# Performance work log

Measured on AMD Instinct MI355X. Metric: run time of the kernel, lower is better.

## Reference

```python
import jax, jax.numpy as jnp
import numpy as np

D = 16      # stroke_embedding_dim
H = 2       # num_heads
DH = D // H # head dim = 8
HID = 32    # hidden_dim
OUT = 32    # output_dim
N = 250000  # num edge nodes
F = 500000  # num faces
E = 4       # edges per face


def setup_inputs() -> dict:
    key = jax.random.key(0)
    ks = jax.random.split(key, 10)
    s = 1.0 / np.sqrt(D)
    return {
        "node_embed": jax.random.normal(ks[0], (1, N, D), dtype=jnp.float32),
        "face_edge_ids": jax.random.randint(ks[1], (F, E), 0, N),
        # nn.MultiheadAttention in_proj (packed q,k,v) and out_proj, stored [in, out]
        "w_in": jax.random.uniform(ks[2], (D, 3 * D), jnp.float32, -s, s),
        "b_in": jnp.zeros((3 * D,), jnp.float32),
        "w_out": jax.random.uniform(ks[3], (D, D), jnp.float32, -s, s),
        "b_out": jnp.zeros((D,), jnp.float32),
        # fc: Linear(16 -> 32), fc_output: Linear(32 -> 32)
        "fc_w": jax.random.uniform(ks[4], (D, HID), jnp.float32, -s, s),
        "fc_b": jax.random.uniform(ks[5], (HID,), jnp.float32, -s, s),
        "fco_w": jax.random.uniform(ks[6], (HID, OUT), jnp.float32, -1 / np.sqrt(HID), 1 / np.sqrt(HID)),
        "fco_b": jax.random.uniform(ks[7], (OUT,), jnp.float32, -1 / np.sqrt(HID), 1 / np.sqrt(HID)),
    }


def reference(node_embed, face_edge_ids, w_in, b_in, w_out, b_out, fc_w, fc_b, fco_w, fco_b):
    # Gather per-face edge embeddings: [F, E, D]
    x = node_embed[0][face_edge_ids]
    # Packed qkv projection
    qkv = x @ w_in + b_in                                  # [F, E, 3D]
    q, k, v = jnp.split(qkv, 3, axis=-1)
    def heads(t):
        return t.reshape(F, E, H, DH).transpose(0, 2, 1, 3)  # [F, H, E, DH]
    q, k, v = heads(q), heads(k), heads(v)
    scores = jnp.einsum("fhqd,fhkd->fhqk", q, k) / np.sqrt(DH)
    attn = jax.nn.softmax(scores, axis=-1)
    o = jnp.einsum("fhqk,fhkd->fhqd", attn, v)             # [F, H, E, DH]
    o = o.transpose(0, 2, 1, 3).reshape(F, E, D)
    attn_out = o @ w_out + b_out                           # [F, E, D]
    h = jax.nn.relu(attn_out @ fc_w + fc_b)                # [F, E, HID]
    pooled = h.mean(axis=1)                                # [F, HID]
    out = pooled @ fco_w + fco_b                           # [F, OUT]
    return out[None]                                       # [1, F, OUT]
```

## Files before the change

kernel.cpp:

```cpp
#include <hip/hip_runtime.h>
#include <stdint.h>


typedef float v2f __attribute__((ext_vector_type(2)));
typedef _Float16 v2h __attribute__((ext_vector_type(2)));
typedef __fp16 h4 __attribute__((ext_vector_type(4)));
typedef float f32x4 __attribute__((ext_vector_type(4)));
typedef uint32_t u32x2 __attribute__((ext_vector_type(2)));
typedef uint32_t u32x4 __attribute__((ext_vector_type(4)));

#define DPP_ROT1 0x39
#define DPP_ROT2 0x4E
#define DPP_ROT3 0x93
#define DPP_XOR1 0xB1

template<int CTRL>
static __device__ __forceinline__ float dppf(float x) {
    return __builtin_bit_cast(float,
        __builtin_amdgcn_mov_dpp(__builtin_bit_cast(int, x), CTRL, 0xF, 0xF, true));
}
template<int CTRL>
static __device__ __forceinline__ v2h dpph(v2h x) {
    return __builtin_bit_cast(v2h,
        __builtin_amdgcn_mov_dpp(__builtin_bit_cast(int, x), CTRL, 0xF, 0xF, true));
}

static __device__ __forceinline__ v2h pkh(float a, float b) {
    v2h r; r.x = (_Float16)a; r.y = (_Float16)b; return r;
}
static __device__ __forceinline__ v2h pkrtz(float a, float b) {
#if __has_builtin(__builtin_amdgcn_cvt_pkrtz)
    return __builtin_bit_cast(v2h, __builtin_amdgcn_cvt_pkrtz(a, b));
#else
    return pkh(a, b);
#endif
}
static __device__ __forceinline__ float fdot2(v2h a, v2h b, float c) {
#if __has_builtin(__builtin_amdgcn_fdot2)
    return __builtin_amdgcn_fdot2(a, b, c, false);
#else
    return fmaf((float)a.x, (float)b.x, fmaf((float)a.y, (float)b.y, c));
#endif
}
static __device__ __forceinline__ v2h fmah(v2h a, v2h b, v2h c) {
    return __builtin_elementwise_fma(a, b, c);
}
static __device__ __forceinline__ v2h ash(uint32_t u) {
    return __builtin_bit_cast(v2h, u);
}
static __device__ __forceinline__ uint32_t bcu(v2h h) {
    return __builtin_bit_cast(uint32_t, h);
}
static __device__ __forceinline__ h4 mkh4(uint32_t lo, uint32_t hi) {
    u32x2 t; t.x = lo; t.y = hi; return __builtin_bit_cast(h4, t);
}
static __device__ __forceinline__ h4 ld2h(const uint32_t* p) {
    u32x2 t; t.x = p[0]; t.y = p[1]; return __builtin_bit_cast(h4, t);
}
static __device__ __forceinline__ f32x4 mfma16(h4 a, h4 b, f32x4 c) {
    return __builtin_amdgcn_mfma_f32_16x16x16f16(a, b, c, 0, 0, 0);
}

template<int CTRL>
static __device__ __forceinline__ void score_rot(const v2h* qh, const v2h* kh,
                                                 float& r0, float& r1) {
    float a0 = 0.f, a1 = 0.f;
#pragma unroll
    for (int d = 0; d < 4; ++d) {
        a0 = fdot2(qh[d],     dpph<CTRL>(kh[d]),     a0);
        a1 = fdot2(qh[4 + d], dpph<CTRL>(kh[4 + d]), a1);
    }
    r0 = a0; r1 = a1;
}
template<int CTRL>
static __device__ __forceinline__ void pv_rot(const v2h* vh, v2h ps0, v2h ps1,
                                              v2h* o) {
#pragma unroll
    for (int d = 0; d < 8; ++d) {
        const v2h vr = dpph<CTRL>(vh[d]);
        o[d] = fmah(d < 4 ? ps0 : ps1, vr, o[d]);
    }
}

static __device__ __forceinline__ void xchg_store(uint32_t* S, int a, int c0,
                                                  int g2, f32x4 c) {
    const float p0 = dppf<DPP_XOR1>(c[0]);
    const float p1 = dppf<DPP_XOR1>(c[1]);
    const float p2 = dppf<DPP_XOR1>(c[2]);
    const float p3 = dppf<DPP_XOR1>(c[3]);
    if ((c0 & 1) == 0) {
        u32x4 w;
        w.x = bcu(pkrtz(c[0], p0));
        w.y = bcu(pkrtz(c[1], p1));
        w.z = bcu(pkrtz(c[2], p2));
        w.w = bcu(pkrtz(c[3], p3));
        *reinterpret_cast<u32x4*>(S + ((c0 >> 1) * 68 + 16 * a + 4 * g2)) = w;
    }
}

__global__ void fold_w(const float* __restrict__ w_in,
                       const float* __restrict__ w_out,
                       const float* __restrict__ b_out,
                       const float* __restrict__ fc_w,
                       const float* __restrict__ fc_b,
                       const float* __restrict__ fco_w,
                       uint32_t* __restrict__ wsu) {
    const int tid = threadIdx.x;
    if (blockIdx.x == 0) {
        if (tid < 384) {
            const int T = tid >> 7, r = tid & 127, l = r >> 1, d = r & 1;
            const int o = 16 * T + (l & 15), k0 = 4 * (l >> 4) + 2 * d;
            wsu[tid] = bcu(pkh(w_in[k0 * 48 + o], w_in[(k0 + 1) * 48 + o]));
        } else if (tid < 640) {
            const int i = tid - 384, b = i >> 7, r = i & 127, l = r >> 1, d = r & 1;
            const int c = 16 * b + (l & 15), k0 = 4 * (l >> 4) + 2 * d;
            float a0 = 0.f, a1 = 0.f;
#pragma unroll
            for (int e = 0; e < 16; ++e) {
                a0 = fmaf(w_out[k0 * 16 + e],       fc_w[e * 32 + c], a0);
                a1 = fmaf(w_out[(k0 + 1) * 16 + e], fc_w[e * 32 + c], a1);
            }
            wsu[tid] = bcu(pkh(a0, a1));
        }
    } else {
        if (tid < 32) {
            float acc = fc_b[tid];
#pragma unroll
            for (int e = 0; e < 16; ++e)
                acc = fmaf(b_out[e], fc_w[e * 32 + tid], acc);
            reinterpret_cast<float*>(wsu)[640 + tid] = acc;
        } else if (tid < 544) {
            const int i = tid - 32;
            const int kt = i >> 8, n = (i >> 7) & 1, r = i & 127, l = r >> 1, d = r & 1;
            const int col = 16 * n + (l & 15), k0 = 16 * kt + 4 * (l >> 4) + 2 * d;
            wsu[672 + i] = bcu(pkh(fco_w[k0 * 32 + col] * 0.25f,
                                   fco_w[(k0 + 1) * 32 + col] * 0.25f));
        }
    }
}

__launch_bounds__(256, 4)
__global__ void face_net(const float* __restrict__ node,
                         const int*   __restrict__ fids,
                         const float* __restrict__ b_in,
                         const uint32_t* __restrict__ wsu,
                         const float* __restrict__ fco_b,
                         float* __restrict__ out, int F) {
    const int l   = threadIdx.x & 63;
    const int wid = threadIdx.x >> 6;
    const int token_base = blockIdx.x * 256 + wid * 64;
    if (token_base >= 4 * F) return;
    const int c0 = l & 15, g2 = l >> 4;

    __shared__ __align__(16) uint8_t lds[4 * 4736];
    uint8_t* wl = lds + wid * 4736;
    uint32_t* S0 = reinterpret_cast<uint32_t*>(wl);
    uint32_t* S1 = reinterpret_cast<uint32_t*>(wl + 2176);

    h4 A[4];
#pragma unroll
    for (int a = 0; a < 4; ++a) {
        const int tok = token_base + 16 * a + c0;
        const int nid = fids[tok];
        const float4 xv = *reinterpret_cast<const float4*>(
            node + (size_t)nid * 16 + g2 * 4);
        A[a] = mkh4(bcu(pkrtz(xv.x, xv.y)), bcu(pkrtz(xv.z, xv.w)));
    }

    const h4 Bq = ld2h(wsu + 0   + l * 2);
    const h4 Bk = ld2h(wsu + 128 + l * 2);
    const float bq = b_in[c0];
    {
        const f32x4 cq0 = {bq, bq, bq, bq};
        const f32x4 ck0 = {0.f, 0.f, 0.f, 0.f};
#pragma unroll
        for (int a = 0; a < 4; ++a) xchg_store(S0, a, c0, g2, mfma16(A[a], Bq, cq0));
#pragma unroll
        for (int a = 0; a < 4; ++a) xchg_store(S1, a, c0, g2, mfma16(A[a], Bk, ck0));
    }

    v2h qh[8], kh[8];
#pragma unroll
    for (int u = 0; u < 4; ++u) {
        qh[2 * u]     = ash(S0[(2 * u) * 68 + l]);
        qh[2 * u + 1] = ash(S0[(2 * u + 1) * 68 + l]);
        kh[2 * u]     = ash(S1[(2 * u) * 68 + l]);
        kh[2 * u + 1] = ash(S1[(2 * u + 1) * 68 + l]);
    }

    float p0[4], p1[4];
    {
        float a0 = 0.f, a1 = 0.f;
#pragma unroll
        for (int d = 0; d < 4; ++d) {
            a0 = fdot2(qh[d], kh[d], a0);
            a1 = fdot2(qh[4 + d], kh[4 + d], a1);
        }
        p0[0] = a0; p1[0] = a1;
    }
    score_rot<DPP_ROT1>(qh, kh, p0[1], p1[1]);
    score_rot<DPP_ROT2>(qh, kh, p0[2], p1[2]);
    score_rot<DPP_ROT3>(qh, kh, p0[3], p1[3]);

    {
        const float C = 0.51006974841f;
        float s0 = 0.f, s1 = 0.f;
#pragma unroll
        for (int j = 0; j < 4; ++j) {
            p0[j] = __builtin_amdgcn_exp2f(p0[j] * C); s0 += p0[j];
            p1[j] = __builtin_amdgcn_exp2f(p1[j] * C); s1 += p1[j];
        }
        const float r0 = __builtin_amdgcn_rcpf(s0);
        const float r1 = __builtin_amdgcn_rcpf(s1);
#pragma unroll
        for (int j = 0; j < 4; ++j) { p0[j] *= r0; p1[j] *= r1; }
    }

    const h4 Bv = ld2h(wsu + 256 + l * 2);
    const float bv = b_in[32 + c0];
    {
        const f32x4 cv0 = {bv, bv, bv, bv};
#pragma unroll
        for (int a = 0; a < 4; ++a) xchg_store(S0, a, c0, g2, mfma16(A[a], Bv, cv0));
    }
    v2h vh[8];
#pragma unroll
    for (int u = 0; u < 4; ++u) {
        vh[2 * u]     = ash(S0[(2 * u) * 68 + l]);
        vh[2 * u + 1] = ash(S0[(2 * u + 1) * 68 + l]);
    }

    v2h ps0[4], ps1[4];
#pragma unroll
    for (int r = 0; r < 4; ++r) {
        ps0[r] = pkrtz(p0[r], p0[r]);
        ps1[r] = pkrtz(p1[r], p1[r]);
    }
    v2h o[8];
#pragma unroll
    for (int d = 0; d < 4; ++d) {
        o[d]     = ps0[0] * vh[d];
        o[4 + d] = ps1[0] * vh[4 + d];
    }
    pv_rot<DPP_ROT1>(vh, ps0[1], ps1[1], o);
    pv_rot<DPP_ROT2>(vh, ps0[2], ps1[2], o);
    pv_rot<DPP_ROT3>(vh, ps0[3], ps1[3], o);

#pragma unroll
    for (int j = 0; j < 4; ++j) {
        u32x2 w; w.x = bcu(o[2 * j]); w.y = bcu(o[2 * j + 1]);
        *reinterpret_cast<u32x2*>(S1 + l * 10 + 2 * j) = w;
    }
    h4 Ao[4];
#pragma unroll
    for (int a = 0; a < 4; ++a) {
        const u32x2 t = *reinterpret_cast<const u32x2*>(
            S1 + (16 * a + c0) * 10 + 2 * g2);
        Ao[a] = __builtin_bit_cast(h4, t);
    }

    const h4 Bh0 = ld2h(wsu + 384 + l * 2);
    const h4 Bh1 = ld2h(wsu + 384 + 128 + l * 2);
    const float* b1f = reinterpret_cast<const float*>(wsu) + 640;
    const float b10 = b1f[c0], b11 = b1f[16 + c0];
    float* Pf = reinterpret_cast<float*>(S0);
    {
        const f32x4 ch0 = {b10, b10, b10, b10};
        const f32x4 ch1 = {b11, b11, b11, b11};
#pragma unroll
        for (int a = 0; a < 4; ++a) {
            const f32x4 h0 = mfma16(Ao[a], Bh0, ch0);
            const f32x4 h1 = mfma16(Ao[a], Bh1, ch1);
            const float s0 = fmaxf(h0[0], 0.f) + fmaxf(h0[1], 0.f)
                           + fmaxf(h0[2], 0.f) + fmaxf(h0[3], 0.f);
            const float s1 = fmaxf(h1[0], 0.f) + fmaxf(h1[1], 0.f)
                           + fmaxf(h1[2], 0.f) + fmaxf(h1[3], 0.f);
            Pf[(4 * a + g2) * 34 + c0]      = s0;
            Pf[(4 * a + g2) * 34 + 16 + c0] = s1;
        }
    }

    h4 Af[2];
#pragma unroll
    for (int kt = 0; kt < 2; ++kt) {
        const u32x2 pa = *reinterpret_cast<const u32x2*>(
            S0 + c0 * 34 + 16 * kt + 4 * g2);
        const u32x2 pb = *reinterpret_cast<const u32x2*>(
            S0 + c0 * 34 + 16 * kt + 4 * g2 + 2);
        const v2f fa = __builtin_bit_cast(v2f, pa);
        const v2f fb = __builtin_bit_cast(v2f, pb);
        Af[kt] = mkh4(bcu(pkrtz(fa.x, fa.y)), bcu(pkrtz(fb.x, fb.y)));
    }
    const h4 Bf00 = ld2h(wsu + 672 + 0 * 128 + l * 2);
    const h4 Bf01 = ld2h(wsu + 672 + 1 * 128 + l * 2);
    const h4 Bf10 = ld2h(wsu + 672 + 2 * 128 + l * 2);
    const h4 Bf11 = ld2h(wsu + 672 + 3 * 128 + l * 2);
    const float fb0 = fco_b[c0], fb1 = fco_b[16 + c0];
    f32x4 cf0 = {fb0, fb0, fb0, fb0};
    f32x4 cf1 = {fb1, fb1, fb1, fb1};
    cf0 = mfma16(Af[0], Bf00, cf0);
    cf0 = mfma16(Af[1], Bf10, cf0);
    cf1 = mfma16(Af[0], Bf01, cf1);
    cf1 = mfma16(Af[1], Bf11, cf1);

    const int fbase = token_base >> 2;
    float* ob = out + (size_t)(fbase + 4 * g2) * 32 + c0;
#pragma unroll
    for (int r = 0; r < 4; ++r) {
        ob[r * 32]      = cf0[r];
        ob[r * 32 + 16] = cf1[r];
    }
}

extern "C" void kernel_launch(void* const* d_in, const int* in_sizes, int n_in,
                              void* d_out, int out_size, void* d_ws, size_t ws_size,
                              hipStream_t stream) {
    const float* node  = (const float*)d_in[0];
    const int*   fids  = (const int*)  d_in[1];
    const float* w_in  = (const float*)d_in[2];
    const float* b_in  = (const float*)d_in[3];
    const float* w_out = (const float*)d_in[4];
    const float* b_out = (const float*)d_in[5];
    const float* fc_w  = (const float*)d_in[6];
    const float* fc_b  = (const float*)d_in[7];
    const float* fco_w = (const float*)d_in[8];
    const float* fco_b = (const float*)d_in[9];
    float* out = (float*)d_out;
    uint32_t* wsu = (uint32_t*)d_ws;
    const int F = in_sizes[1] / 4;

    hipLaunchKernelGGL(fold_w, dim3(2), dim3(640), 0, stream,
                       w_in, w_out, b_out, fc_w, fc_b, fco_w, wsu);
    const int threads = F * 4;
    const int blocks = (threads + 255) / 256;
    hipLaunchKernelGGL(face_net, dim3(blocks), dim3(256), 0, stream,
                       node, fids, b_in, wsu, fco_b, out, F);
}
```

Baseline: 134.9 us.

## Compute attention scores and PV via masked MFMAs, eliminating LDS staging

```diff
diff --git a/kernel.cpp b/kernel.cpp
--- a/kernel.cpp
+++ b/kernel.cpp
@@ -2,26 +2,17 @@
 #include <stdint.h>
 
 
-typedef float v2f __attribute__((ext_vector_type(2)));
 typedef _Float16 v2h __attribute__((ext_vector_type(2)));
 typedef __fp16 h4 __attribute__((ext_vector_type(4)));
 typedef float f32x4 __attribute__((ext_vector_type(4)));
 typedef uint32_t u32x2 __attribute__((ext_vector_type(2)));
-typedef uint32_t u32x4 __attribute__((ext_vector_type(4)));
-
-#define DPP_ROT1 0x39
+
 #define DPP_ROT2 0x4E
-#define DPP_ROT3 0x93
 #define DPP_XOR1 0xB1
 
 template<int CTRL>
 static __device__ __forceinline__ float dppf(float x) {
     return __builtin_bit_cast(float,
-        __builtin_amdgcn_mov_dpp(__builtin_bit_cast(int, x), CTRL, 0xF, 0xF, true));
-}
-template<int CTRL>
-static __device__ __forceinline__ v2h dpph(v2h x) {
-    return __builtin_bit_cast(v2h,
         __builtin_amdgcn_mov_dpp(__builtin_bit_cast(int, x), CTRL, 0xF, 0xF, true));
 }
 
@@ -35,19 +26,6 @@
     return pkh(a, b);
 #endif
 }
-static __device__ __forceinline__ float fdot2(v2h a, v2h b, float c) {
-#if __has_builtin(__builtin_amdgcn_fdot2)
-    return __builtin_amdgcn_fdot2(a, b, c, false);
-#else
-    return fmaf((float)a.x, (float)b.x, fmaf((float)a.y, (float)b.y, c));
-#endif
-}
-static __device__ __forceinline__ v2h fmah(v2h a, v2h b, v2h c) {
-    return __builtin_elementwise_fma(a, b, c);
-}
-static __device__ __forceinline__ v2h ash(uint32_t u) {
-    return __builtin_bit_cast(v2h, u);
-}
 static __device__ __forceinline__ uint32_t bcu(v2h h) {
     return __builtin_bit_cast(uint32_t, h);
 }
@@ -60,42 +38,13 @@
 static __device__ __forceinline__ f32x4 mfma16(h4 a, h4 b, f32x4 c) {
     return __builtin_amdgcn_mfma_f32_16x16x16f16(a, b, c, 0, 0, 0);
 }
-
-template<int CTRL>
-static __device__ __forceinline__ void score_rot(const v2h* qh, const v2h* kh,
-                                                 float& r0, float& r1) {
-    float a0 = 0.f, a1 = 0.f;
-#pragma unroll
-    for (int d = 0; d < 4; ++d) {
-        a0 = fdot2(qh[d],     dpph<CTRL>(kh[d]),     a0);
-        a1 = fdot2(qh[4 + d], dpph<CTRL>(kh[4 + d]), a1);
-    }
-    r0 = a0; r1 = a1;
-}
-template<int CTRL>
-static __device__ __forceinline__ void pv_rot(const v2h* vh, v2h ps0, v2h ps1,
-                                              v2h* o) {
-#pragma unroll
-    for (int d = 0; d < 8; ++d) {
-        const v2h vr = dpph<CTRL>(vh[d]);
-        o[d] = fmah(d < 4 ? ps0 : ps1, vr, o[d]);
-    }
-}
-
-static __device__ __forceinline__ void xchg_store(uint32_t* S, int a, int c0,
-                                                  int g2, f32x4 c) {
-    const float p0 = dppf<DPP_XOR1>(c[0]);
-    const float p1 = dppf<DPP_XOR1>(c[1]);
-    const float p2 = dppf<DPP_XOR1>(c[2]);
-    const float p3 = dppf<DPP_XOR1>(c[3]);
-    if ((c0 & 1) == 0) {
-        u32x4 w;
-        w.x = bcu(pkrtz(c[0], p0));
-        w.y = bcu(pkrtz(c[1], p1));
-        w.z = bcu(pkrtz(c[2], p2));
-        w.w = bcu(pkrtz(c[3], p3));
-        *reinterpret_cast<u32x4*>(S + ((c0 >> 1) * 68 + 16 * a + 4 * g2)) = w;
-    }
+static __device__ __forceinline__ h4 packC(f32x4 c) {
+    return mkh4(bcu(pkrtz(c[0], c[1])), bcu(pkrtz(c[2], c[3])));
+}
+static __device__ __forceinline__ h4 selh(bool keep, h4 x) {
+    u32x2 t = __builtin_bit_cast(u32x2, x);
+    u32x2 r; r.x = keep ? t.x : 0u; r.y = keep ? t.y : 0u;
+    return __builtin_bit_cast(h4, r);
 }
 
 __global__ void fold_w(const float* __restrict__ w_in,
@@ -149,166 +98,109 @@
     const int l   = threadIdx.x & 63;
     const int wid = threadIdx.x >> 6;
     const int token_base = blockIdx.x * 256 + wid * 64;
-    if (token_base >= 4 * F) return;
+    const int total = 4 * F;
+    if (token_base >= total) return;
     const int c0 = l & 15, g2 = l >> 4;
 
-    __shared__ __align__(16) uint8_t lds[4 * 4736];
-    uint8_t* wl = lds + wid * 4736;
-    uint32_t* S0 = reinterpret_cast<uint32_t*>(wl);
-    uint32_t* S1 = reinterpret_cast<uint32_t*>(wl + 2176);
-
-    h4 A[4];
+    h4 X[4];
 #pragma unroll
     for (int a = 0; a < 4; ++a) {
-        const int tok = token_base + 16 * a + c0;
+        int tok = token_base + 16 * a + c0;
+        tok = tok < total ? tok : total - 1;
         const int nid = fids[tok];
         const float4 xv = *reinterpret_cast<const float4*>(
             node + (size_t)nid * 16 + g2 * 4);
-        A[a] = mkh4(bcu(pkrtz(xv.x, xv.y)), bcu(pkrtz(xv.z, xv.w)));
+        X[a] = mkh4(bcu(pkrtz(xv.x, xv.y)), bcu(pkrtz(xv.z, xv.w)));
     }
 
-    const h4 Bq = ld2h(wsu + 0   + l * 2);
-    const h4 Bk = ld2h(wsu + 128 + l * 2);
-    const float bq = b_in[c0];
-    {
-        const f32x4 cq0 = {bq, bq, bq, bq};
-        const f32x4 ck0 = {0.f, 0.f, 0.f, 0.f};
-#pragma unroll
-        for (int a = 0; a < 4; ++a) xchg_store(S0, a, c0, g2, mfma16(A[a], Bq, cq0));
-#pragma unroll
-        for (int a = 0; a < 4; ++a) xchg_store(S1, a, c0, g2, mfma16(A[a], Bk, ck0));
-    }
-
-    v2h qh[8], kh[8];
-#pragma unroll
-    for (int u = 0; u < 4; ++u) {
-        qh[2 * u]     = ash(S0[(2 * u) * 68 + l]);
-        qh[2 * u + 1] = ash(S0[(2 * u + 1) * 68 + l]);
-        kh[2 * u]     = ash(S1[(2 * u) * 68 + l]);
-        kh[2 * u + 1] = ash(S1[(2 * u + 1) * 68 + l]);
-    }
-
-    float p0[4], p1[4];
-    {
-        float a0 = 0.f, a1 = 0.f;
-#pragma unroll
-        for (int d = 0; d < 4; ++d) {
-            a0 = fdot2(qh[d], kh[d], a0);
-            a1 = fdot2(qh[4 + d], kh[4 + d], a1);
-        }
-        p0[0] = a0; p1[0] = a1;
-    }
-    score_rot<DPP_ROT1>(qh, kh, p0[1], p1[1]);
-    score_rot<DPP_ROT2>(qh, kh, p0[2], p1[2]);
-    score_rot<DPP_ROT3>(qh, kh, p0[3], p1[3]);
-
-    {
-        const float C = 0.51006974841f;
-        float s0 = 0.f, s1 = 0.f;
-#pragma unroll
-        for (int j = 0; j < 4; ++j) {
-            p0[j] = __builtin_amdgcn_exp2f(p0[j] * C); s0 += p0[j];
-            p1[j] = __builtin_amdgcn_exp2f(p1[j] * C); s1 += p1[j];
-        }
-        const float r0 = __builtin_amdgcn_rcpf(s0);
-        const float r1 = __builtin_amdgcn_rcpf(s1);
-#pragma unroll
-        for (int j = 0; j < 4; ++j) { p0[j] *= r0; p1[j] *= r1; }
-    }
-
-    const h4 Bv = ld2h(wsu + 256 + l * 2);
-    const float bv = b_in[32 + c0];
-    {
-        const f32x4 cv0 = {bv, bv, bv, bv};
-#pragma unroll
-        for (int a = 0; a < 4; ++a) xchg_store(S0, a, c0, g2, mfma16(A[a], Bv, cv0));
-    }
-    v2h vh[8];
-#pragma unroll
-    for (int u = 0; u < 4; ++u) {
-        vh[2 * u]     = ash(S0[(2 * u) * 68 + l]);
-        vh[2 * u + 1] = ash(S0[(2 * u + 1) * 68 + l]);
-    }
-
-    v2h ps0[4], ps1[4];
-#pragma unroll
-    for (int r = 0; r < 4; ++r) {
-        ps0[r] = pkrtz(p0[r], p0[r]);
-        ps1[r] = pkrtz(p1[r], p1[r]);
-    }
-    v2h o[8];
-#pragma unroll
-    for (int d = 0; d < 4; ++d) {
-        o[d]     = ps0[0] * vh[d];
-        o[4 + d] = ps1[0] * vh[4 + d];
-    }
-    pv_rot<DPP_ROT1>(vh, ps0[1], ps1[1], o);
-    pv_rot<DPP_ROT2>(vh, ps0[2], ps1[2], o);
-    pv_rot<DPP_ROT3>(vh, ps0[3], ps1[3], o);
-
-#pragma unroll
-    for (int j = 0; j < 4; ++j) {
-        u32x2 w; w.x = bcu(o[2 * j]); w.y = bcu(o[2 * j + 1]);
-        *reinterpret_cast<u32x2*>(S1 + l * 10 + 2 * j) = w;
-    }
-    h4 Ao[4];
+    const h4 WqT  = ld2h(wsu + 0   + l * 2);
+    const h4 WkT  = ld2h(wsu + 128 + l * 2);
+    const h4 WvB  = ld2h(wsu + 256 + l * 2);
+    const h4 EhA0 = ld2h(wsu + 384 + l * 2);
+    const h4 EhA1 = ld2h(wsu + 512 + l * 2);
+    const h4 Ef00 = ld2h(wsu + 672 + 0 * 128 + l * 2);
+    const h4 Ef01 = ld2h(wsu + 672 + 1 * 128 + l * 2);
+    const h4 Ef10 = ld2h(wsu + 672 + 2 * 128 + l * 2);
+    const h4 Ef11 = ld2h(wsu + 672 + 3 * 128 + l * 2);
+
+    const float4 bq4 = *reinterpret_cast<const float4*>(b_in + 4 * g2);
+    const float  bv  = b_in[32 + c0];
+    const float* b1f = reinterpret_cast<const float*>(wsu) + 640;
+    const float4 b10 = *reinterpret_cast<const float4*>(b1f + 4 * g2);
+    const float4 b11 = *reinterpret_cast<const float4*>(b1f + 16 + 4 * g2);
+    const float4 fb0 = *reinterpret_cast<const float4*>(fco_b + 4 * g2);
+    const float4 fb1 = *reinterpret_cast<const float4*>(fco_b + 16 + 4 * g2);
+
+    const bool scoreH0 = (g2 < 2);
+    const bool pvH0    = (c0 < 8);
+    const bool valid   = (g2 == (c0 >> 2));
+    const int fbase = token_base >> 2;
+    const float C = 0.51006974841f;
+    const f32x4 zz = {0.f, 0.f, 0.f, 0.f};
+
 #pragma unroll
     for (int a = 0; a < 4; ++a) {
-        const u32x2 t = *reinterpret_cast<const u32x2*>(
-            S1 + (16 * a + c0) * 10 + 2 * g2);
-        Ao[a] = __builtin_bit_cast(h4, t);
-    }
-
-    const h4 Bh0 = ld2h(wsu + 384 + l * 2);
-    const h4 Bh1 = ld2h(wsu + 384 + 128 + l * 2);
-    const float* b1f = reinterpret_cast<const float*>(wsu) + 640;
-    const float b10 = b1f[c0], b11 = b1f[16 + c0];
-    float* Pf = reinterpret_cast<float*>(S0);
-    {
-        const f32x4 ch0 = {b10, b10, b10, b10};
-        const f32x4 ch1 = {b11, b11, b11, b11};
-#pragma unroll
-        for (int a = 0; a < 4; ++a) {
-            const f32x4 h0 = mfma16(Ao[a], Bh0, ch0);
-            const f32x4 h1 = mfma16(Ao[a], Bh1, ch1);
-            const float s0 = fmaxf(h0[0], 0.f) + fmaxf(h0[1], 0.f)
-                           + fmaxf(h0[2], 0.f) + fmaxf(h0[3], 0.f);
-            const float s1 = fmaxf(h1[0], 0.f) + fmaxf(h1[1], 0.f)
-                           + fmaxf(h1[2], 0.f) + fmaxf(h1[3], 0.f);
-            Pf[(4 * a + g2) * 34 + c0]      = s0;
-            Pf[(4 * a + g2) * 34 + 16 + c0] = s1;
-        }
-    }
-
-    h4 Af[2];
-#pragma unroll
-    for (int kt = 0; kt < 2; ++kt) {
-        const u32x2 pa = *reinterpret_cast<const u32x2*>(
-            S0 + c0 * 34 + 16 * kt + 4 * g2);
-        const u32x2 pb = *reinterpret_cast<const u32x2*>(
-            S0 + c0 * 34 + 16 * kt + 4 * g2 + 2);
-        const v2f fa = __builtin_bit_cast(v2f, pa);
-        const v2f fb = __builtin_bit_cast(v2f, pb);
-        Af[kt] = mkh4(bcu(pkrtz(fa.x, fa.y)), bcu(pkrtz(fb.x, fb.y)));
-    }
-    const h4 Bf00 = ld2h(wsu + 672 + 0 * 128 + l * 2);
-    const h4 Bf01 = ld2h(wsu + 672 + 1 * 128 + l * 2);
-    const h4 Bf10 = ld2h(wsu + 672 + 2 * 128 + l * 2);
-    const h4 Bf11 = ld2h(wsu + 672 + 3 * 128 + l * 2);
-    const float fb0 = fco_b[c0], fb1 = fco_b[16 + c0];
-    f32x4 cf0 = {fb0, fb0, fb0, fb0};
-    f32x4 cf1 = {fb1, fb1, fb1, fb1};
-    cf0 = mfma16(Af[0], Bf00, cf0);
-    cf0 = mfma16(Af[1], Bf10, cf0);
-    cf1 = mfma16(Af[0], Bf01, cf1);
-    cf1 = mfma16(Af[1], Bf11, cf1);
-
-    const int fbase = token_base >> 2;
-    float* ob = out + (size_t)(fbase + 4 * g2) * 32 + c0;
-#pragma unroll
-    for (int r = 0; r < 4; ++r) {
-        ob[r * 32]      = cf0[r];
-        ob[r * 32 + 16] = cf1[r];
+        f32x4 cq = {bq4.x, bq4.y, bq4.z, bq4.w};
+        f32x4 cv = {bv, bv, bv, bv};
+        const f32x4 Dq = mfma16(WqT, X[a], cq);
+        const f32x4 Dk = mfma16(WkT, X[a], zz);
+        const f32x4 Dv = mfma16(X[a], WvB, cv);
+        const h4 qB = packC(Dq);
+        const h4 kA = packC(Dk);
+        const h4 vA = packC(Dv);
+
+        const f32x4 S0 = mfma16(selh(scoreH0,  kA), qB, zz);
+        const f32x4 S1 = mfma16(selh(!scoreH0, kA), qB, zz);
+
+        const float e00 = __builtin_amdgcn_exp2f(S0[0] * C);
+        const float e01 = __builtin_amdgcn_exp2f(S0[1] * C);
+        const float e02 = __builtin_amdgcn_exp2f(S0[2] * C);
+        const float e03 = __builtin_amdgcn_exp2f(S0[3] * C);
+        const float e10 = __builtin_amdgcn_exp2f(S1[0] * C);
+        const float e11 = __builtin_amdgcn_exp2f(S1[1] * C);
+        const float e12 = __builtin_amdgcn_exp2f(S1[2] * C);
+        const float e13 = __builtin_amdgcn_exp2f(S1[3] * C);
+        const float r0 = __builtin_amdgcn_rcpf((e00 + e01) + (e02 + e03));
+        const float r1 = __builtin_amdgcn_rcpf((e10 + e11) + (e12 + e13));
+        const h4 PB0 = selh(valid, mkh4(bcu(pkrtz(e00 * r0, e01 * r0)),
+                                        bcu(pkrtz(e02 * r0, e03 * r0))));
+        const h4 PB1 = selh(valid, mkh4(bcu(pkrtz(e10 * r1, e11 * r1)),
+                                        bcu(pkrtz(e12 * r1, e13 * r1))));
+
+        f32x4 Ot = mfma16(selh(pvH0,  vA), PB0, zz);
+        Ot       = mfma16(selh(!pvH0, vA), PB1, Ot);
+        const h4 hB = packC(Ot);
+
+        f32x4 ch0 = {b10.x, b10.y, b10.z, b10.w};
+        f32x4 ch1 = {b11.x, b11.y, b11.z, b11.w};
+        const f32x4 H0 = mfma16(EhA0, hB, ch0);
+        const f32x4 H1 = mfma16(EhA1, hB, ch1);
+        float pool[8];
+#pragma unroll
+        for (int r = 0; r < 4; ++r) {
+            float x0 = fmaxf(H0[r], 0.f);
+            float s0 = x0 + dppf<DPP_XOR1>(x0); s0 = s0 + dppf<DPP_ROT2>(s0);
+            pool[r] = s0;
+            float x1 = fmaxf(H1[r], 0.f);
+            float s1 = x1 + dppf<DPP_XOR1>(x1); s1 = s1 + dppf<DPP_ROT2>(s1);
+            pool[4 + r] = s1;
+        }
+        const h4 pB0 = mkh4(bcu(pkrtz(pool[0], pool[1])),
+                            bcu(pkrtz(pool[2], pool[3])));
+        const h4 pB1 = mkh4(bcu(pkrtz(pool[4], pool[5])),
+                            bcu(pkrtz(pool[6], pool[7])));
+
+        f32x4 cf0 = {fb0.x, fb0.y, fb0.z, fb0.w};
+        f32x4 cf1 = {fb1.x, fb1.y, fb1.z, fb1.w};
+        const f32x4 O0 = mfma16(Ef10, pB1, mfma16(Ef00, pB0, cf0));
+        const f32x4 O1 = mfma16(Ef11, pB1, mfma16(Ef01, pB0, cf1));
+
+        if ((c0 & 3) == 0) {
+            const int face = fbase + 4 * a + (c0 >> 2);
+            float* ob = out + (size_t)face * 32 + 4 * g2;
+            *reinterpret_cast<float4*>(ob)      = make_float4(O0[0], O0[1], O0[2], O0[3]);
+            *reinterpret_cast<float4*>(ob + 16) = make_float4(O1[0], O1[1], O1[2], O1[3]);
+        }
     }
 }
 
```

After: 135.7 us. About the same (+0.6%).
